# Kernel optimization log

Measured on AMD Instinct MI355X. Metric: run time of the kernel, lower is better.

## Reference

```python
import jax, jax.numpy as jnp
import numpy as np

MACRO_CURVE_ORDER = 3
MAX_ACTION_LEN = 24
NUM_CURVES = 8
VOCAB = 361
NUM_LAYERS = 6
HID = 32


def setup_inputs() -> dict:
    key = jax.random.key(0)
    ks = iter(jax.random.split(key, 32))
    B, N_PART, P, CTX = 4096, 100, 64, 64

    def lin(k, din, dout):
        k1, k2 = jax.random.split(k)
        s = 1.0 / np.sqrt(din)
        return (jax.random.uniform(k1, (din, dout), jnp.float32, -s, s),
                jax.random.uniform(k2, (dout,), jnp.float32, -s, s))

    fc1_w, fc1_b = lin(next(ks), P, 256)
    fc2_w, fc2_b = lin(next(ks), 256, 256)
    fc3_w, fc3_b = lin(next(ks), CTX + 256, 512)
    fc4_w, fc4_b = lin(next(ks), 512, 256)
    fc5_w, fc5_b = lin(next(ks), 256, 128)
    fc6_w, fc6_b = lin(next(ks), 128, 32)
    fc10_w, fc10_b = lin(next(ks), HID, VOCAB)

    s = 1.0 / np.sqrt(HID)
    lstm_wih = jax.random.uniform(next(ks), (NUM_LAYERS, HID, 4 * HID), jnp.float32, -s, s)
    lstm_whh = jax.random.uniform(next(ks), (NUM_LAYERS, HID, 4 * HID), jnp.float32, -s, s)
    lstm_bih = jax.random.uniform(next(ks), (NUM_LAYERS, 4 * HID), jnp.float32, -s, s)
    lstm_bhh = jax.random.uniform(next(ks), (NUM_LAYERS, 4 * HID), jnp.float32, -s, s)

    return {
        "c": jax.random.normal(next(ks), (B, CTX), jnp.float32),
        "x": jax.random.normal(next(ks), (B, N_PART * P), jnp.float32),
        "hidden": jnp.zeros((NUM_LAYERS, B, HID), jnp.float32),
        "cell": jnp.zeros((NUM_LAYERS, B, HID), jnp.float32),
        "fc1_w": fc1_w, "fc1_b": fc1_b, "fc2_w": fc2_w, "fc2_b": fc2_b,
        "fc3_w": fc3_w, "fc3_b": fc3_b, "fc4_w": fc4_w, "fc4_b": fc4_b,
        "fc5_w": fc5_w, "fc5_b": fc5_b, "fc6_w": fc6_w, "fc6_b": fc6_b,
        "lstm_wih": lstm_wih, "lstm_whh": lstm_whh,
        "lstm_bih": lstm_bih, "lstm_bhh": lstm_bhh,
        "fc10_w": fc10_w, "fc10_b": fc10_b,
        "particle_size": P,
    }


def _lstm_stack(x, h, c, wih, whh, bih, bhh):
    """One time step through 6 stacked LSTM layers (PyTorch cell math)."""
    hs, cs = [], []
    inp = x
    for l in range(NUM_LAYERS):
        gates = inp @ wih[l] + bih[l] + h[l] @ whh[l] + bhh[l]  # (B, 4*HID)
        i, f, g, o = jnp.split(gates, 4, axis=-1)
        i, f, o = jax.nn.sigmoid(i), jax.nn.sigmoid(f), jax.nn.sigmoid(o)
        g = jnp.tanh(g)
        c_new = f * c[l] + i * g
        h_new = o * jnp.tanh(c_new)
        hs.append(h_new)
        cs.append(c_new)
        inp = h_new
    return inp, jnp.stack(hs), jnp.stack(cs)


def reference(c, x, hidden, cell, fc1_w, fc1_b, fc2_w, fc2_b, fc3_w, fc3_b,
              fc4_w, fc4_b, fc5_w, fc5_b, fc6_w, fc6_b,
              lstm_wih, lstm_whh, lstm_bih, lstm_bhh, fc10_w, fc10_b,
              particle_size):
    B = x.shape[0]
    # Belief (particle) encoder with mean pooling.
    xp = x.reshape(B, -1, particle_size)
    xp = jax.nn.relu(xp @ fc1_w + fc1_b)
    xp = jax.nn.relu(xp @ fc2_w + fc2_b)
    xp = xp.mean(axis=-2)  # (B, 256)
    z = jnp.concatenate([c, xp], axis=-1)
    z = jax.nn.relu(z @ fc3_w + fc3_b)
    z = jax.nn.relu(z @ fc4_w + fc4_b)
    z = jax.nn.relu(z @ fc5_w + fc5_b)
    z = jax.nn.relu(z @ fc6_w + fc6_b)  # (B, 32)

    def step(carry, _):
        xt, h, cst = carry
        xt, h, cst = _lstm_stack(xt, h, cst, lstm_wih, lstm_whh, lstm_bih, lstm_bhh)
        logits = xt @ fc10_w + fc10_b  # (B, VOCAB)
        idx = jax.lax.top_k(logits, NUM_CURVES)[1]  # (B, NUM_CURVES)
        return (xt, h, cst), idx

    (_, _, _), idxs = jax.lax.scan(step, (z, hidden, cell), None, length=MAX_ACTION_LEN)
    # (T, B, K) -> (B, T*K)
    preds = jnp.transpose(idxs, (1, 0, 2)).reshape(B, MAX_ACTION_LEN * NUM_CURVES)
    return preds
```

## Files before the change

kernel.cpp:

```cpp
#include <hip/hip_runtime.h>
#include <math.h>

#define BATCH 4096
#define NPART 100
#define PSZ   64

__device__ __forceinline__ void fma4(float4& d, const float s, const float4 v) {
    d.x = fmaf(s, v.x, d.x); d.y = fmaf(s, v.y, d.y);
    d.z = fmaf(s, v.z, d.z); d.w = fmaf(s, v.w, d.w);
}
__device__ __forceinline__ float4 addrelu4(const float4 a, const float4 b) {
    return make_float4(fmaxf(a.x + b.x, 0.f), fmaxf(a.y + b.y, 0.f),
                       fmaxf(a.z + b.z, 0.f), fmaxf(a.w + b.w, 0.f));
}

template<int NRR>
__device__ __forceinline__ void enc_chunk(
    const float* __restrict__ xb, const int rbase,
    const float* __restrict__ w1c, const float* __restrict__ w2c,
    float* __restrict__ h1s,
    const int rg, const int col0,
    const float4 b1a, const float4 b1b, const float4 b2a, const float4 b2b,
    float* msum)
{
    int rowr[NRR];
    #pragma unroll
    for (int rr = 0; rr < NRR; ++rr)
        rowr[rr] = rbase + ((NRR == 1 && rg >= 4) ? 0 : (rg + 8 * rr));

    float4 a0[NRR], a1[NRR];
    #pragma unroll
    for (int rr = 0; rr < NRR; ++rr) {
        a0[rr] = make_float4(0.f, 0.f, 0.f, 0.f);
        a1[rr] = make_float4(0.f, 0.f, 0.f, 0.f);
    }
    #pragma unroll 2
    for (int k0 = 0; k0 < 64; k0 += 4) {
        float4 bva[4], bvb[4];
        #pragma unroll
        for (int kk = 0; kk < 4; ++kk) {
            bva[kk] = *(const float4*)(w1c + (k0 + kk) * 256);
            bvb[kk] = *(const float4*)(w1c + (k0 + kk) * 256 + 4);
        }
        #pragma unroll
        for (int rr = 0; rr < NRR; ++rr) {
            const float4 av = *(const float4*)(xb + (size_t)rowr[rr] * 64 + k0);
            fma4(a0[rr], av.x, bva[0]); fma4(a0[rr], av.y, bva[1]);
            fma4(a0[rr], av.z, bva[2]); fma4(a0[rr], av.w, bva[3]);
            fma4(a1[rr], av.x, bvb[0]); fma4(a1[rr], av.y, bvb[1]);
            fma4(a1[rr], av.z, bvb[2]); fma4(a1[rr], av.w, bvb[3]);
        }
    }
    #pragma unroll
    for (int rr = 0; rr < NRR; ++rr) {
        const int r = rg + 8 * rr;
        *(float4*)&h1s[r * 260 + col0]     = addrelu4(a0[rr], b1a);
        *(float4*)&h1s[r * 260 + col0 + 4] = addrelu4(a1[rr], b1b);
    }
    __syncthreads();

    float4 c0[NRR], c1[NRR];
    #pragma unroll
    for (int rr = 0; rr < NRR; ++rr) {
        c0[rr] = make_float4(0.f, 0.f, 0.f, 0.f);
        c1[rr] = make_float4(0.f, 0.f, 0.f, 0.f);
    }
    #pragma unroll 2
    for (int k0 = 0; k0 < 256; k0 += 4) {
        float4 bva[4], bvb[4];
        #pragma unroll
        for (int kk = 0; kk < 4; ++kk) {
            bva[kk] = *(const float4*)(w2c + (k0 + kk) * 256);
            bvb[kk] = *(const float4*)(w2c + (k0 + kk) * 256 + 4);
        }
        #pragma unroll
        for (int rr = 0; rr < NRR; ++rr) {
            const float4 av = *(const float4*)&h1s[(rg + 8 * rr) * 260 + k0];
            fma4(c0[rr], av.x, bva[0]); fma4(c0[rr], av.y, bva[1]);
            fma4(c0[rr], av.z, bva[2]); fma4(c0[rr], av.w, bva[3]);
            fma4(c1[rr], av.x, bvb[0]); fma4(c1[rr], av.y, bvb[1]);
            fma4(c1[rr], av.z, bvb[2]); fma4(c1[rr], av.w, bvb[3]);
        }
    }
    #pragma unroll
    for (int rr = 0; rr < NRR; ++rr) {
        if (NRR == 4 || rg < 4) {
            msum[0] += fmaxf(c0[rr].x + b2a.x, 0.f);
            msum[1] += fmaxf(c0[rr].y + b2a.y, 0.f);
            msum[2] += fmaxf(c0[rr].z + b2a.z, 0.f);
            msum[3] += fmaxf(c0[rr].w + b2a.w, 0.f);
            msum[4] += fmaxf(c1[rr].x + b2b.x, 0.f);
            msum[5] += fmaxf(c1[rr].y + b2b.y, 0.f);
            msum[6] += fmaxf(c1[rr].z + b2b.z, 0.f);
            msum[7] += fmaxf(c1[rr].w + b2b.w, 0.f);
        }
    }
    __syncthreads();
}

__global__ __launch_bounds__(256) void k_encoder(
    const float* __restrict__ x,
    const float* __restrict__ w1, const float* __restrict__ b1,
    const float* __restrict__ w2, const float* __restrict__ b2,
    float* __restrict__ xp)
{
    __shared__ __align__(16) float h1s[32 * 260];
    const int tid  = threadIdx.x;
    const int b    = blockIdx.x;
    const int lane = tid & 63;
    const int wv   = tid >> 6;
    const int cgw  = lane & 7;
    const int rg   = lane >> 3;
    const int col0 = wv * 64 + cgw * 8;

    const float* xb  = x + (size_t)b * (NPART * PSZ);
    const float* w1c = w1 + col0;
    const float* w2c = w2 + col0;
    const float4 b1a = *(const float4*)&b1[col0];
    const float4 b1b = *(const float4*)&b1[col0 + 4];
    const float4 b2a = *(const float4*)&b2[col0];
    const float4 b2b = *(const float4*)&b2[col0 + 4];

    float msum[8] = {0.f,0.f,0.f,0.f,0.f,0.f,0.f,0.f};

    enc_chunk<4>(xb,  0, w1c, w2c, h1s, rg, col0, b1a, b1b, b2a, b2b, msum);
    enc_chunk<4>(xb, 32, w1c, w2c, h1s, rg, col0, b1a, b1b, b2a, b2b, msum);
    enc_chunk<4>(xb, 64, w1c, w2c, h1s, rg, col0, b1a, b1b, b2a, b2b, msum);
    enc_chunk<1>(xb, 96, w1c, w2c, h1s, rg, col0, b1a, b1b, b2a, b2b, msum);

    #pragma unroll
    for (int q = 0; q < 8; ++q) {
        msum[q] += __shfl_xor(msum[q], 8, 64);
        msum[q] += __shfl_xor(msum[q], 16, 64);
        msum[q] += __shfl_xor(msum[q], 32, 64);
    }
    if (rg == 0) {
        float4 o0 = make_float4(msum[0] / 100.f, msum[1] / 100.f,
                                msum[2] / 100.f, msum[3] / 100.f);
        float4 o1 = make_float4(msum[4] / 100.f, msum[5] / 100.f,
                                msum[6] / 100.f, msum[7] / 100.f);
        *(float4*)&xp[(size_t)b * 256 + col0]     = o0;
        *(float4*)&xp[(size_t)b * 256 + col0 + 4] = o1;
    }
}

__global__ __launch_bounds__(256) void k_mlp(
    const float* __restrict__ cin, const float* __restrict__ xp,
    const float* __restrict__ w3, const float* __restrict__ b3,
    const float* __restrict__ w4, const float* __restrict__ b4,
    const float* __restrict__ w5, const float* __restrict__ b5,
    const float* __restrict__ w6, const float* __restrict__ b6,
    float* __restrict__ z)
{
    __shared__ float in0[8][320];
    __shared__ float h3[8][512];
    __shared__ float h4[8][256];
    __shared__ float h5[8][128];
    const int tid  = threadIdx.x;
    const int row0 = blockIdx.x * 8;

    for (int i = tid; i < 8 * 16; i += 256) {
        int r = i >> 4, q = i & 15;
        *(float4*)&in0[r][q * 4] = *(const float4*)&cin[(size_t)(row0 + r) * 64 + q * 4];
    }
    for (int i = tid; i < 8 * 64; i += 256) {
        int r = i >> 6, q = i & 63;
        *(float4*)&in0[r][64 + q * 4] = *(const float4*)&xp[(size_t)(row0 + r) * 256 + q * 4];
    }
    __syncthreads();

    {
        float a0[8], a1[8];
        #pragma unroll
        for (int r = 0; r < 8; ++r) { a0[r] = 0.f; a1[r] = 0.f; }
        const int c0 = tid, c1 = tid + 256;
        for (int kq = 0; kq < 80; ++kq) {
            const int k0 = kq * 4;
            float wa0 = w3[(k0+0)*512 + c0], wa1 = w3[(k0+1)*512 + c0];
            float wa2 = w3[(k0+2)*512 + c0], wa3 = w3[(k0+3)*512 + c0];
            float wb0 = w3[(k0+0)*512 + c1], wb1 = w3[(k0+1)*512 + c1];
            float wb2 = w3[(k0+2)*512 + c1], wb3 = w3[(k0+3)*512 + c1];
            #pragma unroll
            for (int r = 0; r < 8; ++r) {
                const float4 a = *(const float4*)&in0[r][k0];
                a0[r] = fmaf(a.x, wa0, fmaf(a.y, wa1, fmaf(a.z, wa2, fmaf(a.w, wa3, a0[r]))));
                a1[r] = fmaf(a.x, wb0, fmaf(a.y, wb1, fmaf(a.z, wb2, fmaf(a.w, wb3, a1[r]))));
            }
        }
        const float bb0 = b3[c0], bb1 = b3[c1];
        #pragma unroll
        for (int r = 0; r < 8; ++r) {
            h3[r][c0] = fmaxf(a0[r] + bb0, 0.f);
            h3[r][c1] = fmaxf(a1[r] + bb1, 0.f);
        }
    }
    __syncthreads();

    {
        float ac[8];
        #pragma unroll
        for (int r = 0; r < 8; ++r) ac[r] = 0.f;
        for (int kq = 0; kq < 128; ++kq) {
            const int k0 = kq * 4;
            float w0 = w4[(k0+0)*256 + tid], w1v = w4[(k0+1)*256 + tid];
            float w2v = w4[(k0+2)*256 + tid], w3v = w4[(k0+3)*256 + tid];
            #pragma unroll
            for (int r = 0; r < 8; ++r) {
                const float4 a = *(const float4*)&h3[r][k0];
                ac[r] = fmaf(a.x, w0, fmaf(a.y, w1v, fmaf(a.z, w2v, fmaf(a.w, w3v, ac[r]))));
            }
        }
        const float bb = b4[tid];
        #pragma unroll
        for (int r = 0; r < 8; ++r) h4[r][tid] = fmaxf(ac[r] + bb, 0.f);
    }
    __syncthreads();

    {
        const int c5 = tid & 127, half = tid >> 7;
        float ac[4];
        #pragma unroll
        for (int r = 0; r < 4; ++r) ac[r] = 0.f;
        for (int kq = 0; kq < 64; ++kq) {
            const int k0 = kq * 4;
            float w0 = w5[(k0+0)*128 + c5], w1v = w5[(k0+1)*128 + c5];
            float w2v = w5[(k0+2)*128 + c5], w3v = w5[(k0+3)*128 + c5];
            #pragma unroll
            for (int r = 0; r < 4; ++r) {
                const float4 a = *(const float4*)&h4[half * 4 + r][k0];
                ac[r] = fmaf(a.x, w0, fmaf(a.y, w1v, fmaf(a.z, w2v, fmaf(a.w, w3v, ac[r]))));
            }
        }
        const float bb = b5[c5];
        #pragma unroll
        for (int r = 0; r < 4; ++r) h5[half * 4 + r][c5] = fmaxf(ac[r] + bb, 0.f);
    }
    __syncthreads();

    {
        const int c6 = tid & 31, r = tid >> 5;
        float ac = 0.f;
        for (int kq = 0; kq < 32; ++kq) {
            const int k0 = kq * 4;
            float w0 = w6[(k0+0)*32 + c6], w1v = w6[(k0+1)*32 + c6];
            float w2v = w6[(k0+2)*32 + c6], w3v = w6[(k0+3)*32 + c6];
            const float4 a = *(const float4*)&h5[r][k0];
            ac = fmaf(a.x, w0, fmaf(a.y, w1v, fmaf(a.z, w2v, fmaf(a.w, w3v, ac))));
        }
        z[(size_t)(row0 + r) * 32 + c6] = fmaxf(ac + b6[c6], 0.f);
    }
}

__global__ __launch_bounds__(256) void k_lstm(
    const float* __restrict__ z,
    const float* __restrict__ hid0, const float* __restrict__ cel0,
    const float* __restrict__ wih, const float* __restrict__ whh,
    const float* __restrict__ bih, const float* __restrict__ bhh,
    const float* __restrict__ w10, const float* __restrict__ b10,
    int* __restrict__ out)
{
    __shared__ float xs[8][32];
    __shared__ float hs[6][8][32];
    __shared__ float cs[6][8][32];
    __shared__ float gates[8][128];
    __shared__ float logits[8][361];
    const int tid  = threadIdx.x;
    const int row0 = blockIdx.x * 8;

    for (int i = tid; i < 8 * 32; i += 256) xs[0][i] = z[(size_t)row0 * 32 + i];
    for (int i = tid; i < 6 * 8 * 32; i += 256) {
        int l = i >> 8, rj = i & 255;
        (&hs[0][0][0])[i] = hid0[(size_t)l * BATCH * 32 + (size_t)row0 * 32 + rj];
        (&cs[0][0][0])[i] = cel0[(size_t)l * BATCH * 32 + (size_t)row0 * 32 + rj];
    }
    __syncthreads();

    const int g  = tid & 127, rg = tid >> 7;
    const int jc = tid & 31,  jr = tid >> 5;
    const int wv = tid >> 6,  lane = tid & 63;

    for (int t = 0; t < 24; ++t) {
        for (int l = 0; l < 6; ++l) {
            const float* inp = (l == 0) ? ((t == 0) ? &xs[0][0] : &hs[5][0][0])
                                        : &hs[l - 1][0][0];
            const float* WI = wih + (size_t)l * 32 * 128;
            const float* WH = whh + (size_t)l * 32 * 128;
            const float bsum = bih[l * 128 + g] + bhh[l * 128 + g];
            float acc[4] = {bsum, bsum, bsum, bsum};
            #pragma unroll
            for (int k = 0; k < 32; k += 4) {
                float wi0 = WI[(k+0)*128 + g], wi1 = WI[(k+1)*128 + g];
                float wi2 = WI[(k+2)*128 + g], wi3 = WI[(k+3)*128 + g];
                float wh0 = WH[(k+0)*128 + g], wh1 = WH[(k+1)*128 + g];
                float wh2 = WH[(k+2)*128 + g], wh3 = WH[(k+3)*128 + g];
                #pragma unroll
                for (int rr = 0; rr < 4; ++rr) {
                    const int r = rg * 4 + rr;
                    const float4 ai = *(const float4*)&inp[r * 32 + k];
                    const float4 ah = *(const float4*)&hs[l][r][k];
                    acc[rr] = fmaf(ai.x, wi0, acc[rr]); acc[rr] = fmaf(ai.y, wi1, acc[rr]);
                    acc[rr] = fmaf(ai.z, wi2, acc[rr]); acc[rr] = fmaf(ai.w, wi3, acc[rr]);
                    acc[rr] = fmaf(ah.x, wh0, acc[rr]); acc[rr] = fmaf(ah.y, wh1, acc[rr]);
                    acc[rr] = fmaf(ah.z, wh2, acc[rr]); acc[rr] = fmaf(ah.w, wh3, acc[rr]);
                }
            }
            #pragma unroll
            for (int rr = 0; rr < 4; ++rr) gates[rg * 4 + rr][g] = acc[rr];
            __syncthreads();

            {
                const float gi = gates[jr][jc],      gf = gates[jr][32 + jc];
                const float gg = gates[jr][64 + jc], go = gates[jr][96 + jc];
                const float i_ = 1.f / (1.f + expf(-gi));
                const float f_ = 1.f / (1.f + expf(-gf));
                const float o_ = 1.f / (1.f + expf(-go));
                const float g_ = tanhf(gg);
                const float cn = f_ * cs[l][jr][jc] + i_ * g_;
                cs[l][jr][jc] = cn;
                hs[l][jr][jc] = o_ * tanhf(cn);
            }
            __syncthreads();
        }

        #pragma unroll
        for (int pass = 0; pass < 2; ++pass) {
            const int v = tid + pass * 256;
            if (v < 361) {
                const float bb = b10[v];
                float a8[8];
                #pragma unroll
                for (int r = 0; r < 8; ++r) a8[r] = bb;
                #pragma unroll
                for (int k = 0; k < 32; k += 4) {
                    float w0 = w10[(k+0)*361 + v], w1v = w10[(k+1)*361 + v];
                    float w2v = w10[(k+2)*361 + v], w3v = w10[(k+3)*361 + v];
                    #pragma unroll
                    for (int r = 0; r < 8; ++r) {
                        const float4 a = *(const float4*)&hs[5][r][k];
                        a8[r] = fmaf(a.x, w0, fmaf(a.y, w1v, fmaf(a.z, w2v, fmaf(a.w, w3v, a8[r]))));
                    }
                }
                #pragma unroll
                for (int r = 0; r < 8; ++r) logits[r][v] = a8[r];
            }
        }
        __syncthreads();

        for (int rr = 0; rr < 2; ++rr) {
            const int r = wv * 2 + rr;
            float val[6];
            #pragma unroll
            for (int s = 0; s < 6; ++s) {
                const int v = lane + 64 * s;
                val[s] = (v < 361) ? logits[r][v] : -3.4e38f;
            }
            unsigned msk = 0x3Fu;
            const int rowg = row0 + r;
            for (int sel = 0; sel < 8; ++sel) {
                float bv = -3.4e38f; int bi = 0x7FFFFFFF;
                #pragma unroll
                for (int s = 0; s < 6; ++s) {
                    if (msk & (1u << s)) {
                        const float v2 = val[s]; const int i2 = lane + 64 * s;
                        if (v2 > bv || (v2 == bv && i2 < bi)) { bv = v2; bi = i2; }
                    }
                }
                #pragma unroll
                for (int off = 32; off >= 1; off >>= 1) {
                    const float ov = __shfl_xor(bv, off, 64);
                    const int   oi = __shfl_xor(bi, off, 64);
                    if (ov > bv || (ov == bv && oi < bi)) { bv = ov; bi = oi; }
                }
                if ((bi & 63) == lane) msk &= ~(1u << (bi >> 6));
                if (lane == 0) out[(size_t)rowg * 192 + t * 8 + sel] = bi;
            }
        }
        __syncthreads();
    }
}

extern "C" void kernel_launch(void* const* d_in, const int* in_sizes, int n_in,
                              void* d_out, int out_size, void* d_ws, size_t ws_size,
                              hipStream_t stream) {
    const float* cin  = (const float*)d_in[0];
    const float* x    = (const float*)d_in[1];
    const float* hid0 = (const float*)d_in[2];
    const float* cel0 = (const float*)d_in[3];
    const float* w1 = (const float*)d_in[4];  const float* b1 = (const float*)d_in[5];
    const float* w2 = (const float*)d_in[6];  const float* b2 = (const float*)d_in[7];
    const float* w3 = (const float*)d_in[8];  const float* b3 = (const float*)d_in[9];
    const float* w4 = (const float*)d_in[10]; const float* b4 = (const float*)d_in[11];
    const float* w5 = (const float*)d_in[12]; const float* b5 = (const float*)d_in[13];
    const float* w6 = (const float*)d_in[14]; const float* b6 = (const float*)d_in[15];
    const float* wih = (const float*)d_in[16]; const float* whh = (const float*)d_in[17];
    const float* bih = (const float*)d_in[18]; const float* bhh = (const float*)d_in[19];
    const float* w10 = (const float*)d_in[20]; const float* b10 = (const float*)d_in[21];

    float* xp = (float*)d_ws;
    float* zz = xp + (size_t)BATCH * 256;
    int*   out = (int*)d_out;

    k_encoder<<<BATCH, 256, 0, stream>>>(x, w1, b1, w2, b2, xp);
    k_mlp<<<BATCH / 8, 256, 0, stream>>>(cin, xp, w3, b3, w4, b4, w5, b5, w6, b6, zz);
    k_lstm<<<BATCH / 8, 256, 0, stream>>>(zz, hid0, cel0, wih, whh, bih, bhh, w10, b10, out);
}
```

Before: 2.401 ms.

## Stage fc2 weight panels into LDS via double-buffered async global_load_lds

The second encoder GEMM now reads fc2 weights from shared memory instead of issuing per-thread global float4 loads. The weights are copied in 16-row panels with the gfx950 global-to-LDS direct load and double-buffered, so the next panel's copy overlaps the FMAs on the current one. This removes repeated L1/L2 weight traffic from each wave. In exchange it adds 32 KB of LDS per block, which may cut occupancy, and adds a barrier per panel. It also depends on the compiler inserting the right vmcnt waits for the async copies.

```diff
diff --git a/kernel.cpp b/kernel.cpp
--- a/kernel.cpp
+++ b/kernel.cpp
@@ -14,15 +14,33 @@
                        fmaxf(a.z + b.z, 0.f), fmaxf(a.w + b.w, 0.f));
 }
 
+typedef const __attribute__((address_space(1))) unsigned int  gu32;
+typedef __attribute__((address_space(3)))       unsigned int  lu32;
+__device__ __forceinline__ void gload_lds16(const float* g, float* l) {
+    __builtin_amdgcn_global_load_lds((gu32*)g, (lu32*)l, 16, 0, 0);
+}
+
+__device__ __forceinline__ void stage_panel(const float* __restrict__ w2,
+                                            float* dst, const int p,
+                                            const int wv, const int lane) {
+    const float* g = w2 + p * (16 * 256) + wv * 256 + lane * 4;
+    float*       l = dst + wv * 256;
+    #pragma unroll
+    for (int s = 0; s < 4; ++s)
+        gload_lds16(g + s * 1024, l + s * 1024);
+}
+
 template<int NRR>
 __device__ __forceinline__ void enc_chunk(
     const float* __restrict__ xb, const int rbase,
-    const float* __restrict__ w1c, const float* __restrict__ w2c,
-    float* __restrict__ h1s,
-    const int rg, const int col0,
+    const float* __restrict__ w1c, const float* __restrict__ w2,
+    float* __restrict__ h1s, float* __restrict__ wpan,
+    const int wv, const int lane, const int rg, const int col0,
     const float4 b1a, const float4 b1b, const float4 b2a, const float4 b2b,
     float* msum)
 {
+    stage_panel(w2, wpan, 0, wv, lane);
+
     int rowr[NRR];
     #pragma unroll
     for (int rr = 0; rr < NRR; ++rr)
@@ -65,23 +83,33 @@
         c0[rr] = make_float4(0.f, 0.f, 0.f, 0.f);
         c1[rr] = make_float4(0.f, 0.f, 0.f, 0.f);
     }
-    #pragma unroll 2
-    for (int k0 = 0; k0 < 256; k0 += 4) {
-        float4 bva[4], bvb[4];
-        #pragma unroll
-        for (int kk = 0; kk < 4; ++kk) {
-            bva[kk] = *(const float4*)(w2c + (k0 + kk) * 256);
-            bvb[kk] = *(const float4*)(w2c + (k0 + kk) * 256 + 4);
-        }
-        #pragma unroll
-        for (int rr = 0; rr < NRR; ++rr) {
-            const float4 av = *(const float4*)&h1s[(rg + 8 * rr) * 260 + k0];
-            fma4(c0[rr], av.x, bva[0]); fma4(c0[rr], av.y, bva[1]);
-            fma4(c0[rr], av.z, bva[2]); fma4(c0[rr], av.w, bva[3]);
-            fma4(c1[rr], av.x, bvb[0]); fma4(c1[rr], av.y, bvb[1]);
-            fma4(c1[rr], av.z, bvb[2]); fma4(c1[rr], av.w, bvb[3]);
-        }
-    }
+    #pragma unroll 1
+    for (int p = 0; p < 16; ++p) {
+        if (p < 15)
+            stage_panel(w2, wpan + ((p + 1) & 1) * (16 * 256), p + 1, wv, lane);
+        const float* wp = wpan + (p & 1) * (16 * 256);
+        #pragma unroll
+        for (int it = 0; it < 4; ++it) {
+            const int kk0 = it * 4;
+            float4 bva[4], bvb[4];
+            #pragma unroll
+            for (int kk = 0; kk < 4; ++kk) {
+                bva[kk] = *(const float4*)&wp[(kk0 + kk) * 256 + col0];
+                bvb[kk] = *(const float4*)&wp[(kk0 + kk) * 256 + col0 + 4];
+            }
+            const int kg = p * 16 + kk0;
+            #pragma unroll
+            for (int rr = 0; rr < NRR; ++rr) {
+                const float4 av = *(const float4*)&h1s[(rg + 8 * rr) * 260 + kg];
+                fma4(c0[rr], av.x, bva[0]); fma4(c0[rr], av.y, bva[1]);
+                fma4(c0[rr], av.z, bva[2]); fma4(c0[rr], av.w, bva[3]);
+                fma4(c1[rr], av.x, bvb[0]); fma4(c1[rr], av.y, bvb[1]);
+                fma4(c1[rr], av.z, bvb[2]); fma4(c1[rr], av.w, bvb[3]);
+            }
+        }
+        __syncthreads();
+    }
+
     #pragma unroll
     for (int rr = 0; rr < NRR; ++rr) {
         if (NRR == 4 || rg < 4) {
@@ -95,7 +123,6 @@
             msum[7] += fmaxf(c1[rr].w + b2b.w, 0.f);
         }
     }
-    __syncthreads();
 }
 
 __global__ __launch_bounds__(256) void k_encoder(
@@ -105,6 +132,7 @@
     float* __restrict__ xp)
 {
     __shared__ __align__(16) float h1s[32 * 260];
+    __shared__ __align__(16) float wpan[2 * 16 * 256];
     const int tid  = threadIdx.x;
     const int b    = blockIdx.x;
     const int lane = tid & 63;
@@ -115,7 +143,6 @@
 
     const float* xb  = x + (size_t)b * (NPART * PSZ);
     const float* w1c = w1 + col0;
-    const float* w2c = w2 + col0;
     const float4 b1a = *(const float4*)&b1[col0];
     const float4 b1b = *(const float4*)&b1[col0 + 4];
     const float4 b2a = *(const float4*)&b2[col0];
@@ -123,10 +150,10 @@
 
     float msum[8] = {0.f,0.f,0.f,0.f,0.f,0.f,0.f,0.f};
 
-    enc_chunk<4>(xb,  0, w1c, w2c, h1s, rg, col0, b1a, b1b, b2a, b2b, msum);
-    enc_chunk<4>(xb, 32, w1c, w2c, h1s, rg, col0, b1a, b1b, b2a, b2b, msum);
-    enc_chunk<4>(xb, 64, w1c, w2c, h1s, rg, col0, b1a, b1b, b2a, b2b, msum);
-    enc_chunk<1>(xb, 96, w1c, w2c, h1s, rg, col0, b1a, b1b, b2a, b2b, msum);
+    enc_chunk<4>(xb,  0, w1c, w2, h1s, wpan, wv, lane, rg, col0, b1a, b1b, b2a, b2b, msum);
+    enc_chunk<4>(xb, 32, w1c, w2, h1s, wpan, wv, lane, rg, col0, b1a, b1b, b2a, b2b, msum);
+    enc_chunk<4>(xb, 64, w1c, w2, h1s, wpan, wv, lane, rg, col0, b1a, b1b, b2a, b2b, msum);
+    enc_chunk<1>(xb, 96, w1c, w2, h1s, wpan, wv, lane, rg, col0, b1a, b1b, b2a, b2b, msum);
 
     #pragma unroll
     for (int q = 0; q < 8; ++q) {
```

New measurement: 2.191 ms. -8.8%, faster.
